# Optimization experiments

Measured on AMD Instinct MI355X. Metric: run time of the kernel, lower is better.

## Reference

```python
import jax, jax.numpy as jnp
import numpy as np

C = 256      # channels
G = 8        # groups
K = 9        # 3x3 sampling points (DCNv4 default kernel_size=3)
DWK = 3      # dw_kernel_size (wrapper passes kernel_size=3)
OFFSET_SCALE = 1.0
N, H, W = 8, 64, 64


def setup_inputs() -> dict:
    key = jax.random.key(0)
    ks = jax.random.split(key, 6)
    def init(k, shape, fan):
        return jax.random.normal(k, shape, jnp.float32) * (fan ** -0.5)
    return {
        "x": jax.random.normal(ks[0], (N, C, H, W), jnp.float32),
        "dw_w": init(ks[1], (C, 1, DWK, DWK), DWK * DWK),   # depthwise conv (OIHW, groups=C)
        "dw_b": jnp.zeros((C,), jnp.float32),
        "om_w": init(ks[2], (G * K * 3, C), C) * 0.01,       # offset/mask linear (small offsets)
        "om_b": jnp.zeros((G * K * 3,), jnp.float32),
        "vp_w": init(ks[3], (C, C), C),                      # value_proj
        "vp_b": jnp.zeros((C,), jnp.float32),
        "op_w": init(ks[4], (C, C), C),                      # output_proj (output_bias=False)
    }


def reference(x, dw_w, dw_b, om_w, om_b, vp_w, vp_b, op_w):
    n, c, h, w = x.shape
    cg = c // G
    L = h * w
    # b c h w -> b (h w) c
    xf = x.transpose(0, 2, 3, 1).reshape(n, L, c)
    value = (xf @ vp_w.T + vp_b).reshape(n, L, G, cg)
    # offset/mask branch: depthwise conv on raw input, then linear
    om_in = jax.lax.conv_general_dilated(
        x, dw_w, (1, 1), "SAME", feature_group_count=c,
        dimension_numbers=("NCHW", "OIHW", "NCHW")) + dw_b[None, :, None, None]
    om = om_in.transpose(0, 2, 3, 1).reshape(n, L, c) @ om_w.T + om_b  # (n, L, G*K*3)
    om = om.reshape(n, h, w, G, K * 3)
    off = om[..., : 2 * K].reshape(n, h, w, G, K, 2) * OFFSET_SCALE     # (dy, dx) per point
    mask = om[..., 2 * K:]                                              # (n,h,w,G,K) raw (DCNv4: no softmax)
    # base 3x3 dilation-1 grid centered at each pixel
    d = jnp.arange(-1, 2, dtype=jnp.float32)
    dy, dx = jnp.meshgrid(d, d, indexing="ij")
    base = jnp.stack([dy.ravel(), dx.ravel()], -1)  # (K, 2)
    py = (jnp.arange(h, dtype=jnp.float32).reshape(1, h, 1, 1, 1)
          + base[:, 0].reshape(1, 1, 1, 1, K) + off[..., 0])  # (n,h,w,G,K)
    px = (jnp.arange(w, dtype=jnp.float32).reshape(1, 1, w, 1, 1)
          + base[:, 1].reshape(1, 1, 1, 1, K) + off[..., 1])
    y0 = jnp.floor(py); x0 = jnp.floor(px)
    ty = py - y0; tx = px - x0
    y0i = y0.astype(jnp.int32); x0i = x0.astype(jnp.int32)

    def gather(yi, xi, wgt):
        valid = (yi >= 0) & (yi < h) & (xi >= 0) & (xi < w)
        idx = jnp.clip(yi, 0, h - 1) * w + jnp.clip(xi, 0, w - 1)       # (n,h,w,G,K)
        idx = idx.transpose(0, 1, 2, 4, 3).reshape(n, L * K, G)[..., None]
        g = jnp.take_along_axis(value, idx, axis=1)                     # (n, L*K, G, cg)
        g = g.reshape(n, h, w, K, G, cg).transpose(0, 1, 2, 4, 3, 5)    # (n,h,w,G,K,cg)
        return g * (wgt * valid)[..., None]

    sampled = (gather(y0i,     x0i,     (1 - ty) * (1 - tx))
             + gather(y0i,     x0i + 1, (1 - ty) * tx)
             + gather(y0i + 1, x0i,     ty * (1 - tx))
             + gather(y0i + 1, x0i + 1, ty * tx))
    out = jnp.einsum("nhwgk,nhwgkc->nhwgc", mask, sampled)  # mask-weighted aggregation
    out = out.reshape(n, L, c) @ op_w.T                      # output_proj (no bias)
    # b (h w) c -> b c h w
    return out.reshape(n, h, w, c).transpose(0, 3, 1, 2)
```

## Files before the change

kernel.cpp:

```cpp
#include <hip/hip_runtime.h>
#include <math.h>

#define N_  8
#define C_  256
#define G_  8
#define CG_ 32
#define K_  9
#define H_  64
#define W_  64
#define L_  (H_*W_)
#define OM_ 216
#define OMP_ 256

using frag_ab = __attribute__((ext_vector_type(8))) short;
using frag_cd = __attribute__((ext_vector_type(4))) float;

__device__ __forceinline__ unsigned short f2bf(float f) {
    unsigned int u = __float_as_uint(f);
    u += 0x7FFFu + ((u >> 16) & 1u);
    return (unsigned short)(u >> 16);
}
__device__ __forceinline__ float bflo(unsigned int u) { return __uint_as_float(u << 16); }
__device__ __forceinline__ float bfhi(unsigned int u) { return __uint_as_float(u & 0xFFFF0000u); }

__device__ __forceinline__ void gld16(const void* g, void* l) {
    __builtin_amdgcn_global_load_lds((const __attribute__((address_space(1))) void*)g,
                                     (__attribute__((address_space(3))) void*)l, 16, 0, 0);
}

__global__ __launch_bounds__(256) void prep_kernel(const float* __restrict__ x,
                                                   const float* __restrict__ w,
                                                   const float* __restrict__ b,
                                                   const float* __restrict__ vp_w,
                                                   const float* __restrict__ om_w,
                                                   const float* __restrict__ om_b,
                                                   const float* __restrict__ op_w,
                                                   unsigned short* __restrict__ xb,
                                                   unsigned short* __restrict__ omb,
                                                   unsigned short* __restrict__ vp_wb,
                                                   unsigned short* __restrict__ om_wb,
                                                   float* __restrict__ om_bp,
                                                   unsigned short* __restrict__ op_wb) {
    const int n = blockIdx.z, y = blockIdx.y, c0 = blockIdx.x * 32;
    const int tid = threadIdx.x;
    __shared__ float xs[3][32][66];
    __shared__ __align__(16) unsigned short os[2][64][40];
    if (tid < 192) {
        int r = tid / 64, c = (tid / 2) % 32, e = tid & 1;
        xs[r][c][e * 65] = 0.f;
    }
    const float* xbase = x + ((size_t)n * C_ + c0) * L_;
    for (int i = tid; i < 3 * 32 * 16; i += 256) {
        int r = i >> 9, rem = i & 511, c = rem >> 4, x4 = (rem & 15) * 4;
        int yy = y + r - 1;
        float4 v = make_float4(0.f, 0.f, 0.f, 0.f);
        if ((unsigned)yy < (unsigned)H_) v = *(const float4*)(xbase + (size_t)c * L_ + yy * W_ + x4);
        xs[r][c][1 + x4] = v.x; xs[r][c][2 + x4] = v.y;
        xs[r][c][3 + x4] = v.z; xs[r][c][4 + x4] = v.w;
    }
    __syncthreads();

    const int c = tid & 31, x0 = (tid >> 5) * 8;
    float wv[9];
#pragma unroll
    for (int i = 0; i < 9; i++) wv[i] = w[(c0 + c) * 9 + i];
    const float bias = b[c0 + c];
    float o[8];
#pragma unroll
    for (int j = 0; j < 8; j++) o[j] = bias;
#pragma unroll
    for (int r = 0; r < 3; r++) {
        float v[10];
#pragma unroll
        for (int d = 0; d < 10; d++) v[d] = xs[r][c][x0 + d];
#pragma unroll
        for (int j = 0; j < 8; j++)
            o[j] += wv[r * 3] * v[j] + wv[r * 3 + 1] * v[j + 1] + wv[r * 3 + 2] * v[j + 2];
    }
#pragma unroll
    for (int j = 0; j < 8; j++) {
        os[0][x0 + j][c] = f2bf(xs[1][c][1 + x0 + j]);
        os[1][x0 + j][c] = f2bf(o[j]);
    }
    __syncthreads();

    const int l = tid >> 2, c8 = (tid & 3) * 8;
    uint4 va = *(const uint4*)&os[0][l][c8];
    uint4 vc = *(const uint4*)&os[1][l][c8];
    size_t dst = (((size_t)n * 8 + blockIdx.x) * L_ + y * W_ + l) * 32 + c8;
    *(uint4*)(xb + dst) = va;
    *(uint4*)(omb + dst) = vc;

    if (n == 0) {
        int idx = (blockIdx.x + 8 * blockIdx.y) * 256 + tid;
        if (idx < C_ * C_) {
            vp_wb[idx] = f2bf(vp_w[idx]);
            op_wb[idx] = f2bf(op_w[idx]);
            om_wb[idx] = (idx < OM_ * C_) ? f2bf(om_w[idx]) : (unsigned short)0;
        }
        if (idx < OMP_) om_bp[idx] = (idx < OM_) ? om_b[idx] : 0.f;
    }
}

__global__ __launch_bounds__(256) void gemm12_kernel(const unsigned short* __restrict__ xb,
                                                     const unsigned short* __restrict__ omb,
                                                     const unsigned short* __restrict__ vp_wb,
                                                     const unsigned short* __restrict__ om_wb,
                                                     const float* __restrict__ vp_b,
                                                     const float* __restrict__ om_bp,
                                                     unsigned short* __restrict__ valueb,
                                                     float* __restrict__ omf) {
    __shared__ unsigned short As[128 * 32];
    __shared__ unsigned short Bs[128 * 32];
    const int which = blockIdx.z;
    const unsigned short* A = which ? omb : xb;
    const unsigned short* B = which ? om_wb : vp_wb;
    const float* bias = which ? om_bp : vp_b;
    const int tid = threadIdx.x;
    const long i0 = (long)blockIdx.x * 128;
    const long j0 = (long)blockIdx.y * 128;
    const int nA = (int)(i0 >> 12);
    const int lofs = (int)(i0 & 4095);
    const unsigned short* Bb = B + j0 * C_;
    const int wave = tid >> 6, lane = tid & 63;
    const int iw = (wave & 1) * 64, jw = (wave >> 1) * 64;
    const int lm = lane & 15, kq = lane >> 4;
    const int srow = tid >> 2, scol = (tid & 3) * 8;

    frag_cd acc[4][4];
#pragma unroll
    for (int a = 0; a < 4; a++)
#pragma unroll
        for (int c = 0; c < 4; c++) acc[a][c] = (frag_cd){0.f, 0.f, 0.f, 0.f};

    for (int k0 = 0; k0 < C_; k0 += 32) {
        const unsigned short* ga0 = A + (((size_t)nA * 8 + (k0 >> 5)) * L_ + lofs + srow) * 32 + scol;
        const unsigned short* gb0 = Bb + (long)srow * C_ + k0 + scol;
        gld16(ga0,            As + tid * 8);
        gld16(ga0 + 64 * 32,  As + 2048 + tid * 8);
        gld16(gb0,            Bs + tid * 8);
        gld16(gb0 + 64 * C_,  Bs + 2048 + tid * 8);
        __syncthreads();
        frag_ab af[4], bfr[4];
#pragma unroll
        for (int mi = 0; mi < 4; mi++)
            af[mi] = *(const frag_ab*)&As[(iw + mi * 16 + lm) * 32 + kq * 8];
#pragma unroll
        for (int ni = 0; ni < 4; ni++)
            bfr[ni] = *(const frag_ab*)&Bs[(jw + ni * 16 + lm) * 32 + kq * 8];
#pragma unroll
        for (int mi = 0; mi < 4; mi++)
#pragma unroll
            for (int ni = 0; ni < 4; ni++)
                acc[mi][ni] = __builtin_amdgcn_mfma_f32_16x16x32_bf16(af[mi], bfr[ni], acc[mi][ni], 0, 0, 0);
        __syncthreads();
    }

    float bv[4];
#pragma unroll
    for (int ni = 0; ni < 4; ni++)
        bv[ni] = bias[(int)(j0 + jw + ni * 16 + lm)];

    const long ibase = i0 + iw + kq * 4;
    const long jbase = j0 + jw + lm;
#pragma unroll
    for (int mi = 0; mi < 4; mi++) {
#pragma unroll
        for (int ni = 0; ni < 4; ni++) {
            long j = jbase + ni * 16;
#pragma unroll
            for (int r = 0; r < 4; r++) {
                long i = ibase + mi * 16 + r;
                float v = acc[mi][ni][r] + bv[ni];
                if (which)
                    omf[i * OMP_ + j] = v;
                else
                    valueb[i * C_ + j] = f2bf(v);
            }
        }
    }
}

__global__ __launch_bounds__(256, 2) void samplegemm_kernel(const unsigned short* __restrict__ value,
                                                            const float* __restrict__ om,
                                                            const unsigned short* __restrict__ opw,
                                                            float* __restrict__ out) {
    const int n = blockIdx.y, l0 = blockIdx.x * 64;
    const int tid = threadIdx.x;
    __shared__ __align__(16) unsigned short interm[64 * 256];
    __shared__ float4 wgt[64][9];
    __shared__ uint4  soff[64][9];

    const char* vbase = (const char*)(value + (size_t)n * L_ * C_);
    const int lp = tid >> 2;
    const int g = lp & 7;
    const int c8i = tid & 3;
    const int slot = tid & 31;
    const char* vb = vbase + (size_t)(g * CG_ + c8i * 8) * 2;

    for (int rep = 0; rep < 8; rep++) {
        __syncthreads();
        for (int it = tid; it < 576; it += 256) {
            int pl = it / 9, k = it - pl * 9;
            int p = rep * 8 + (pl >> 3), gg = pl & 7;
            int l = l0 + p, y = l >> 6, xp2 = l & 63;
            const float* so = om + ((size_t)n * L_ + l) * OMP_ + gg * 27;
            float offy = so[2 * k], offx = so[2 * k + 1], mk = so[18 + k];
            float py = (float)(y + k / 3 - 1) + offy;
            float px = (float)(xp2 + k % 3 - 1) + offx;
            float fy = floorf(py), fx = floorf(px);
            float ty = py - fy, tx = px - fx;
            int y0 = (int)fy, x0i = (int)fx;
            int y1 = y0 + 1, x1 = x0i + 1;
            float vy0 = ((unsigned)y0 < (unsigned)H_) ? 1.f : 0.f;
            float vy1 = ((unsigned)y1 < (unsigned)H_) ? 1.f : 0.f;
            float vx0 = ((unsigned)x0i < (unsigned)W_) ? 1.f : 0.f;
            float vx1 = ((unsigned)x1 < (unsigned)W_) ? 1.f : 0.f;
            int cy0 = min(max(y0, 0), H_ - 1), cy1 = min(max(y1, 0), H_ - 1);
            int cx0 = min(max(x0i, 0), W_ - 1), cx1 = min(max(x1, 0), W_ - 1);
            wgt[pl][k] = make_float4(mk * (1.f - ty) * (1.f - tx) * vy0 * vx0,
                                     mk * (1.f - ty) * tx         * vy0 * vx1,
                                     mk * ty         * (1.f - tx) * vy1 * vx0,
                                     mk * ty         * tx         * vy1 * vx1);
            soff[pl][k] = make_uint4((unsigned)((cy0 * W_ + cx0) << 9),
                                     (unsigned)((cy0 * W_ + cx1) << 9),
                                     (unsigned)((cy1 * W_ + cx0) << 9),
                                     (unsigned)((cy1 * W_ + cx1) << 9));
        }
        __syncthreads();
        const int p = rep * 8 + (lp >> 3);
        float acc[8] = {0.f, 0.f, 0.f, 0.f, 0.f, 0.f, 0.f, 0.f};
#pragma unroll
        for (int k = 0; k < K_; k++) {
            float4 wk = wgt[lp][k];
            uint4  ok = soff[lp][k];
            const uint4 v00 = *(const uint4*)(vb + ok.x);
            const uint4 v01 = *(const uint4*)(vb + ok.y);
            const uint4 v10 = *(const uint4*)(vb + ok.z);
            const uint4 v11 = *(const uint4*)(vb + ok.w);
#define ACC8(V, WW) { \
            acc[0] += WW * bflo(V.x); acc[1] += WW * bfhi(V.x); \
            acc[2] += WW * bflo(V.y); acc[3] += WW * bfhi(V.y); \
            acc[4] += WW * bflo(V.z); acc[5] += WW * bfhi(V.z); \
            acc[6] += WW * bflo(V.w); acc[7] += WW * bfhi(V.w); }
            ACC8(v00, wk.x) ACC8(v01, wk.y) ACC8(v10, wk.z) ACC8(v11, wk.w)
#undef ACC8
        }
        uint4 pk;
        unsigned short* ps = (unsigned short*)&pk;
#pragma unroll
        for (int i = 0; i < 8; i++) ps[i] = f2bf(acc[i]);
        int phys = slot ^ (p & 7);
        *(uint4*)&interm[p * 256 + phys * 8] = pk;
    }
    __syncthreads();

    const int wave = tid >> 6, lane = tid & 63;
    const int lm = lane & 15, kq = lane >> 4;
    const int q0w = wave * 64;
    frag_cd acc2[4][4];
#pragma unroll
    for (int a = 0; a < 4; a++)
#pragma unroll
        for (int c = 0; c < 4; c++) acc2[a][c] = (frag_cd){0.f, 0.f, 0.f, 0.f};

    for (int k0 = 0; k0 < C_; k0 += 32) {
        frag_ab af[4], bfr[4];
#pragma unroll
        for (int mi = 0; mi < 4; mi++)
            af[mi] = *(const frag_ab*)(opw + (size_t)(q0w + mi * 16 + lm) * C_ + k0 + kq * 8);
#pragma unroll
        for (int ni = 0; ni < 4; ni++) {
            int pxr = ni * 16 + lm;
            int phys = (k0 / 8 + kq) ^ (pxr & 7);
            bfr[ni] = *(const frag_ab*)&interm[pxr * 256 + phys * 8];
        }
#pragma unroll
        for (int mi = 0; mi < 4; mi++)
#pragma unroll
            for (int ni = 0; ni < 4; ni++)
                acc2[mi][ni] = __builtin_amdgcn_mfma_f32_16x16x32_bf16(af[mi], bfr[ni], acc2[mi][ni], 0, 0, 0);
    }

    float* ob = out + (size_t)n * C_ * L_ + l0;
#pragma unroll
    for (int mi = 0; mi < 4; mi++) {
#pragma unroll
        for (int ni = 0; ni < 4; ni++) {
            int pxr = ni * 16 + lm;
#pragma unroll
            for (int r = 0; r < 4; r++) {
                int q = q0w + mi * 16 + kq * 4 + r;
                ob[(size_t)q * L_ + pxr] = acc2[mi][ni][r];
            }
        }
    }
}

extern "C" void kernel_launch(void* const* d_in, const int* in_sizes, int n_in,
                              void* d_out, int out_size, void* d_ws, size_t ws_size,
                              hipStream_t stream) {
    const float* x    = (const float*)d_in[0];
    const float* dw_w = (const float*)d_in[1];
    const float* dw_b = (const float*)d_in[2];
    const float* om_w = (const float*)d_in[3];
    const float* om_b = (const float*)d_in[4];
    const float* vp_w = (const float*)d_in[5];
    const float* vp_b = (const float*)d_in[6];
    const float* op_w = (const float*)d_in[7];
    float* out = (float*)d_out;

    char* ws = (char*)d_ws;
    unsigned short* xb      = (unsigned short*)(ws);
    unsigned short* omb     = (unsigned short*)(ws + 16777216);
    unsigned short* valueb  = (unsigned short*)(ws + 33554432);
    float*          omf     = (float*)(ws + 50331648);
    unsigned short* vp_wb   = (unsigned short*)(ws + 83886080);
    unsigned short* om_wb   = (unsigned short*)(ws + 84017152);
    unsigned short* op_wb   = (unsigned short*)(ws + 84148224);
    float*          om_bp   = (float*)(ws + 84279296);

    prep_kernel<<<dim3(C_ / 32, H_, N_), 256, 0, stream>>>(
        x, dw_w, dw_b, vp_w, om_w, om_b, op_w,
        xb, omb, vp_wb, om_wb, om_bp, op_wb);
    gemm12_kernel<<<dim3(256, 2, 2), 256, 0, stream>>>(
        xb, omb, vp_wb, om_wb, vp_b, om_bp, valueb, omf);
    samplegemm_kernel<<<dim3(L_ / 64, N_), 256, 0, stream>>>(valueb, omf, op_wb, out);
}
```

Measured before the change: 168.8 us.

## Double sampling threads per block, split bilinear corners, prefetch offsets, swap grid

The sampling+output-projection kernel moves from 256 to 512 threads. Each pixel-group-channel slot now uses two threads, each gathering two of the four bilinear corners, and the partial sums are combined with a lane shuffle. The offset/mask loads for the next rep are prefetched into registers while the current rep is gathered. The MFMA stage is split across 8 waves, each producing 32 output channels. The grid is reordered so batch index is the fast dimension, which changes how blocks are scheduled and may affect L2 locality. The aim is more memory-level parallelism and latency hiding for the gathers, at the cost of more shuffles and less work per wave in the GEMM.

```diff
diff --git a/kernel.cpp b/kernel.cpp
--- a/kernel.cpp
+++ b/kernel.cpp
@@ -26,6 +26,31 @@
 __device__ __forceinline__ void gld16(const void* g, void* l) {
     __builtin_amdgcn_global_load_lds((const __attribute__((address_space(1))) void*)g,
                                      (__attribute__((address_space(3))) void*)l, 16, 0, 0);
+}
+
+__device__ __forceinline__ void tapcalc(int l, int k, float offy, float offx, float mk,
+                                        float4& wq, uint4& sq) {
+    const int y = l >> 6, xp = l & 63;
+    float py = (float)(y + k / 3 - 1) + offy;
+    float px = (float)(xp + k % 3 - 1) + offx;
+    float fy = floorf(py), fx = floorf(px);
+    float ty = py - fy, tx = px - fx;
+    int y0 = (int)fy, x0i = (int)fx;
+    int y1 = y0 + 1, x1 = x0i + 1;
+    float vy0 = ((unsigned)y0 < (unsigned)H_) ? 1.f : 0.f;
+    float vy1 = ((unsigned)y1 < (unsigned)H_) ? 1.f : 0.f;
+    float vx0 = ((unsigned)x0i < (unsigned)W_) ? 1.f : 0.f;
+    float vx1 = ((unsigned)x1 < (unsigned)W_) ? 1.f : 0.f;
+    int cy0 = min(max(y0, 0), H_ - 1), cy1 = min(max(y1, 0), H_ - 1);
+    int cx0 = min(max(x0i, 0), W_ - 1), cx1 = min(max(x1, 0), W_ - 1);
+    wq = make_float4(mk * (1.f - ty) * (1.f - tx) * vy0 * vx0,
+                     mk * (1.f - ty) * tx         * vy0 * vx1,
+                     mk * ty         * (1.f - tx) * vy1 * vx0,
+                     mk * ty         * tx         * vy1 * vx1);
+    sq = make_uint4((unsigned)((cy0 * W_ + cx0) << 9),
+                    (unsigned)((cy0 * W_ + cx1) << 9),
+                    (unsigned)((cy1 * W_ + cx0) << 9),
+                    (unsigned)((cy1 * W_ + cx1) << 9));
 }
 
 __global__ __launch_bounds__(256) void prep_kernel(const float* __restrict__ x,
@@ -181,93 +206,100 @@
     }
 }
 
-__global__ __launch_bounds__(256, 2) void samplegemm_kernel(const unsigned short* __restrict__ value,
+__global__ __launch_bounds__(512, 4) void samplegemm_kernel(const unsigned short* __restrict__ value,
                                                             const float* __restrict__ om,
                                                             const unsigned short* __restrict__ opw,
                                                             float* __restrict__ out) {
-    const int n = blockIdx.y, l0 = blockIdx.x * 64;
+    const int n = blockIdx.x, l0 = blockIdx.y * 64;
     const int tid = threadIdx.x;
     __shared__ __align__(16) unsigned short interm[64 * 256];
     __shared__ float4 wgt[64][9];
     __shared__ uint4  soff[64][9];
 
     const char* vbase = (const char*)(value + (size_t)n * L_ * C_);
-    const int lp = tid >> 2;
+    const int lp = tid >> 3;
     const int g = lp & 7;
-    const int c8i = tid & 3;
-    const int slot = tid & 31;
+    const int pin = lp >> 3;
+    const int sub = tid & 7;
+    const int c8i = sub & 3;
+    const int half = sub >> 2;
+    const int slot = g * 4 + c8i;
     const char* vb = vbase + (size_t)(g * CG_ + c8i * 8) * 2;
+
+    const int itA = tid, plA = itA / 9, kA = itA - plA * 9;
+    const int itB = 512 + tid, plB = itB / 9, kB = itB - plB * 9;
+    const float* omn = om + (size_t)n * L_ * OMP_;
+    const float* soA0 = omn + (size_t)(l0 + (plA >> 3)) * OMP_ + (plA & 7) * 27;
+    const float* soB0 = omn + (size_t)(l0 + (plB >> 3)) * OMP_ + (plB & 7) * 27;
+
+    float aAy = soA0[2 * kA], aAx = soA0[2 * kA + 1], aAm = soA0[18 + kA];
+    float aBy = 0.f, aBx = 0.f, aBm = 0.f;
+    if (tid < 64) { aBy = soB0[2 * kB]; aBx = soB0[2 * kB + 1]; aBm = soB0[18 + kB]; }
 
     for (int rep = 0; rep < 8; rep++) {
         __syncthreads();
-        for (int it = tid; it < 576; it += 256) {
-            int pl = it / 9, k = it - pl * 9;
-            int p = rep * 8 + (pl >> 3), gg = pl & 7;
-            int l = l0 + p, y = l >> 6, xp2 = l & 63;
-            const float* so = om + ((size_t)n * L_ + l) * OMP_ + gg * 27;
-            float offy = so[2 * k], offx = so[2 * k + 1], mk = so[18 + k];
-            float py = (float)(y + k / 3 - 1) + offy;
-            float px = (float)(xp2 + k % 3 - 1) + offx;
-            float fy = floorf(py), fx = floorf(px);
-            float ty = py - fy, tx = px - fx;
-            int y0 = (int)fy, x0i = (int)fx;
-            int y1 = y0 + 1, x1 = x0i + 1;
-            float vy0 = ((unsigned)y0 < (unsigned)H_) ? 1.f : 0.f;
-            float vy1 = ((unsigned)y1 < (unsigned)H_) ? 1.f : 0.f;
-            float vx0 = ((unsigned)x0i < (unsigned)W_) ? 1.f : 0.f;
-            float vx1 = ((unsigned)x1 < (unsigned)W_) ? 1.f : 0.f;
-            int cy0 = min(max(y0, 0), H_ - 1), cy1 = min(max(y1, 0), H_ - 1);
-            int cx0 = min(max(x0i, 0), W_ - 1), cx1 = min(max(x1, 0), W_ - 1);
-            wgt[pl][k] = make_float4(mk * (1.f - ty) * (1.f - tx) * vy0 * vx0,
-                                     mk * (1.f - ty) * tx         * vy0 * vx1,
-                                     mk * ty         * (1.f - tx) * vy1 * vx0,
-                                     mk * ty         * tx         * vy1 * vx1);
-            soff[pl][k] = make_uint4((unsigned)((cy0 * W_ + cx0) << 9),
-                                     (unsigned)((cy0 * W_ + cx1) << 9),
-                                     (unsigned)((cy1 * W_ + cx0) << 9),
-                                     (unsigned)((cy1 * W_ + cx1) << 9));
+        {
+            float4 wq; uint4 sq;
+            tapcalc(l0 + rep * 8 + (plA >> 3), kA, aAy, aAx, aAm, wq, sq);
+            wgt[plA][kA] = wq; soff[plA][kA] = sq;
+            if (tid < 64) {
+                tapcalc(l0 + rep * 8 + (plB >> 3), kB, aBy, aBx, aBm, wq, sq);
+                wgt[plB][kB] = wq; soff[plB][kB] = sq;
+            }
         }
         __syncthreads();
-        const int p = rep * 8 + (lp >> 3);
+        if (rep < 7) {
+            const float* soA = soA0 + (size_t)(rep + 1) * 8 * OMP_;
+            aAy = soA[2 * kA]; aAx = soA[2 * kA + 1]; aAm = soA[18 + kA];
+            if (tid < 64) {
+                const float* soB = soB0 + (size_t)(rep + 1) * 8 * OMP_;
+                aBy = soB[2 * kB]; aBx = soB[2 * kB + 1]; aBm = soB[18 + kB];
+            }
+        }
+        const int p = rep * 8 + pin;
         float acc[8] = {0.f, 0.f, 0.f, 0.f, 0.f, 0.f, 0.f, 0.f};
 #pragma unroll
         for (int k = 0; k < K_; k++) {
             float4 wk = wgt[lp][k];
             uint4  ok = soff[lp][k];
-            const uint4 v00 = *(const uint4*)(vb + ok.x);
-            const uint4 v01 = *(const uint4*)(vb + ok.y);
-            const uint4 v10 = *(const uint4*)(vb + ok.z);
-            const uint4 v11 = *(const uint4*)(vb + ok.w);
+            unsigned oA = half ? ok.z : ok.x; float wA = half ? wk.z : wk.x;
+            unsigned oB = half ? ok.w : ok.y; float wB = half ? wk.w : wk.y;
+            const uint4 vA = *(const uint4*)(vb + oA);
+            const uint4 vB = *(const uint4*)(vb + oB);
 #define ACC8(V, WW) { \
             acc[0] += WW * bflo(V.x); acc[1] += WW * bfhi(V.x); \
             acc[2] += WW * bflo(V.y); acc[3] += WW * bfhi(V.y); \
             acc[4] += WW * bflo(V.z); acc[5] += WW * bfhi(V.z); \
             acc[6] += WW * bflo(V.w); acc[7] += WW * bfhi(V.w); }
-            ACC8(v00, wk.x) ACC8(v01, wk.y) ACC8(v10, wk.z) ACC8(v11, wk.w)
+            ACC8(vA, wA) ACC8(vB, wB)
 #undef ACC8
         }
-        uint4 pk;
-        unsigned short* ps = (unsigned short*)&pk;
-#pragma unroll
-        for (int i = 0; i < 8; i++) ps[i] = f2bf(acc[i]);
-        int phys = slot ^ (p & 7);
-        *(uint4*)&interm[p * 256 + phys * 8] = pk;
+#pragma unroll
+        for (int i = 0; i < 8; i++) acc[i] += __shfl_xor(acc[i], 4);
+        if (half == 0) {
+            uint4 pk;
+            unsigned short* ps = (unsigned short*)&pk;
+#pragma unroll
+            for (int i = 0; i < 8; i++) ps[i] = f2bf(acc[i]);
+            int phys = slot ^ (p & 7);
+            *(uint4*)&interm[p * 256 + phys * 8] = pk;
+        }
     }
     __syncthreads();
 
     const int wave = tid >> 6, lane = tid & 63;
     const int lm = lane & 15, kq = lane >> 4;
-    const int q0w = wave * 64;
-    frag_cd acc2[4][4];
-#pragma unroll
-    for (int a = 0; a < 4; a++)
+    const int q0w = wave * 32;
+    frag_cd acc2[2][4];
+#pragma unroll
+    for (int a = 0; a < 2; a++)
 #pragma unroll
         for (int c = 0; c < 4; c++) acc2[a][c] = (frag_cd){0.f, 0.f, 0.f, 0.f};
 
     for (int k0 = 0; k0 < C_; k0 += 32) {
-        frag_ab af[4], bfr[4];
-#pragma unroll
-        for (int mi = 0; mi < 4; mi++)
+        frag_ab af[2], bfr[4];
+#pragma unroll
+        for (int mi = 0; mi < 2; mi++)
             af[mi] = *(const frag_ab*)(opw + (size_t)(q0w + mi * 16 + lm) * C_ + k0 + kq * 8);
 #pragma unroll
         for (int ni = 0; ni < 4; ni++) {
@@ -276,7 +308,7 @@
             bfr[ni] = *(const frag_ab*)&interm[pxr * 256 + phys * 8];
         }
 #pragma unroll
-        for (int mi = 0; mi < 4; mi++)
+        for (int mi = 0; mi < 2; mi++)
 #pragma unroll
             for (int ni = 0; ni < 4; ni++)
                 acc2[mi][ni] = __builtin_amdgcn_mfma_f32_16x16x32_bf16(af[mi], bfr[ni], acc2[mi][ni], 0, 0, 0);
@@ -284,7 +316,7 @@
 
     float* ob = out + (size_t)n * C_ * L_ + l0;
 #pragma unroll
-    for (int mi = 0; mi < 4; mi++) {
+    for (int mi = 0; mi < 2; mi++) {
 #pragma unroll
         for (int ni = 0; ni < 4; ni++) {
             int pxr = ni * 16 + lm;
@@ -325,5 +357,5 @@
         xb, omb, vp_wb, om_wb, om_bp, op_wb);
     gemm12_kernel<<<dim3(256, 2, 2), 256, 0, stream>>>(
         xb, omb, vp_wb, om_wb, vp_b, om_bp, valueb, omf);
-    samplegemm_kernel<<<dim3(L_ / 64, N_), 256, 0, stream>>>(valueb, omf, op_wb, out);
-}
+    samplegemm_kernel<<<dim3(N_, L_ / 64), 512, 0, stream>>>(valueb, omf, op_wb, out);
+}
```

New measurement: 195.5 us. +15.9%, slower.

## Process four rows per prep block and swap sample kernel grid order

Applied to the files above, without the earlier changes.

The depthwise-conv prep kernel now handles four output rows per block, loading six halo rows once instead of three rows per single output row. This cuts redundant halo reads and block count. The sample/GEMM kernel grid is transposed so that consecutive blocks cover different batches at the same spatial tile, which changes L2 locality and scheduling order. The weight conversion loop is adjusted to cover all entries with the smaller grid.

```diff
diff --git a/kernel.cpp b/kernel.cpp
--- a/kernel.cpp
+++ b/kernel.cpp
@@ -41,18 +41,18 @@
                                                    unsigned short* __restrict__ om_wb,
                                                    float* __restrict__ om_bp,
                                                    unsigned short* __restrict__ op_wb) {
-    const int n = blockIdx.z, y = blockIdx.y, c0 = blockIdx.x * 32;
+    const int n = blockIdx.z, y0 = blockIdx.y * 4, c0 = blockIdx.x * 32;
     const int tid = threadIdx.x;
-    __shared__ float xs[3][32][66];
+    __shared__ float xs[6][32][66];
     __shared__ __align__(16) unsigned short os[2][64][40];
-    if (tid < 192) {
-        int r = tid / 64, c = (tid / 2) % 32, e = tid & 1;
+    for (int i = tid; i < 384; i += 256) {
+        int r = i / 64, c = (i / 2) % 32, e = i & 1;
         xs[r][c][e * 65] = 0.f;
     }
     const float* xbase = x + ((size_t)n * C_ + c0) * L_;
-    for (int i = tid; i < 3 * 32 * 16; i += 256) {
+    for (int i = tid; i < 6 * 32 * 16; i += 256) {
         int r = i >> 9, rem = i & 511, c = rem >> 4, x4 = (rem & 15) * 4;
-        int yy = y + r - 1;
+        int yy = y0 + r - 1;
         float4 v = make_float4(0.f, 0.f, 0.f, 0.f);
         if ((unsigned)yy < (unsigned)H_) v = *(const float4*)(xbase + (size_t)c * L_ + yy * W_ + x4);
         xs[r][c][1 + x4] = v.x; xs[r][c][2 + x4] = v.y;
@@ -65,40 +65,45 @@
 #pragma unroll
     for (int i = 0; i < 9; i++) wv[i] = w[(c0 + c) * 9 + i];
     const float bias = b[c0 + c];
-    float o[8];
-#pragma unroll
-    for (int j = 0; j < 8; j++) o[j] = bias;
-#pragma unroll
-    for (int r = 0; r < 3; r++) {
-        float v[10];
-#pragma unroll
-        for (int d = 0; d < 10; d++) v[d] = xs[r][c][x0 + d];
-#pragma unroll
-        for (int j = 0; j < 8; j++)
-            o[j] += wv[r * 3] * v[j] + wv[r * 3 + 1] * v[j + 1] + wv[r * 3 + 2] * v[j + 2];
-    }
-#pragma unroll
-    for (int j = 0; j < 8; j++) {
-        os[0][x0 + j][c] = f2bf(xs[1][c][1 + x0 + j]);
-        os[1][x0 + j][c] = f2bf(o[j]);
-    }
-    __syncthreads();
-
     const int l = tid >> 2, c8 = (tid & 3) * 8;
-    uint4 va = *(const uint4*)&os[0][l][c8];
-    uint4 vc = *(const uint4*)&os[1][l][c8];
-    size_t dst = (((size_t)n * 8 + blockIdx.x) * L_ + y * W_ + l) * 32 + c8;
-    *(uint4*)(xb + dst) = va;
-    *(uint4*)(omb + dst) = vc;
+
+    for (int rr = 0; rr < 4; rr++) {
+        float o[8];
+#pragma unroll
+        for (int j = 0; j < 8; j++) o[j] = bias;
+#pragma unroll
+        for (int r = 0; r < 3; r++) {
+            float v[10];
+#pragma unroll
+            for (int d = 0; d < 10; d++) v[d] = xs[rr + r][c][x0 + d];
+#pragma unroll
+            for (int j = 0; j < 8; j++)
+                o[j] += wv[r * 3] * v[j] + wv[r * 3 + 1] * v[j + 1] + wv[r * 3 + 2] * v[j + 2];
+        }
+#pragma unroll
+        for (int j = 0; j < 8; j++) {
+            os[0][x0 + j][c] = f2bf(xs[rr + 1][c][1 + x0 + j]);
+            os[1][x0 + j][c] = f2bf(o[j]);
+        }
+        __syncthreads();
+        uint4 va = *(const uint4*)&os[0][l][c8];
+        uint4 vc = *(const uint4*)&os[1][l][c8];
+        size_t dst = (((size_t)n * 8 + blockIdx.x) * L_ + (y0 + rr) * W_ + l) * 32 + c8;
+        *(uint4*)(xb + dst) = va;
+        *(uint4*)(omb + dst) = vc;
+        __syncthreads();
+    }
 
     if (n == 0) {
-        int idx = (blockIdx.x + 8 * blockIdx.y) * 256 + tid;
-        if (idx < C_ * C_) {
+        int base = (blockIdx.x + 8 * blockIdx.y) * 256 + tid;
+#pragma unroll
+        for (int rep2 = 0; rep2 < 2; rep2++) {
+            int idx = base + rep2 * 32768;
             vp_wb[idx] = f2bf(vp_w[idx]);
             op_wb[idx] = f2bf(op_w[idx]);
             om_wb[idx] = (idx < OM_ * C_) ? f2bf(om_w[idx]) : (unsigned short)0;
         }
-        if (idx < OMP_) om_bp[idx] = (idx < OM_) ? om_b[idx] : 0.f;
+        if (base < OMP_) om_bp[base] = (base < OM_) ? om_b[base] : 0.f;
     }
 }
 
@@ -185,7 +190,7 @@
                                                             const float* __restrict__ om,
                                                             const unsigned short* __restrict__ opw,
                                                             float* __restrict__ out) {
-    const int n = blockIdx.y, l0 = blockIdx.x * 64;
+    const int n = blockIdx.x, l0 = blockIdx.y * 64;
     const int tid = threadIdx.x;
     __shared__ __align__(16) unsigned short interm[64 * 256];
     __shared__ float4 wgt[64][9];
@@ -320,10 +325,10 @@
     unsigned short* op_wb   = (unsigned short*)(ws + 84148224);
     float*          om_bp   = (float*)(ws + 84279296);
 
-    prep_kernel<<<dim3(C_ / 32, H_, N_), 256, 0, stream>>>(
+    prep_kernel<<<dim3(C_ / 32, H_ / 4, N_), 256, 0, stream>>>(
         x, dw_w, dw_b, vp_w, om_w, om_b, op_w,
         xb, omb, vp_wb, om_wb, om_bp, op_wb);
     gemm12_kernel<<<dim3(256, 2, 2), 256, 0, stream>>>(
         xb, omb, vp_wb, om_wb, vp_b, om_bp, valueb, omf);
-    samplegemm_kernel<<<dim3(L_ / 64, N_), 256, 0, stream>>>(valueb, omf, op_wb, out);
-}
+    samplegemm_kernel<<<dim3(N_, L_ / 64), 256, 0, stream>>>(valueb, omf, op_wb, out);
+}
```

New measurement: 174.1 us. 3.2% more time.
